# Kernel optimization log

Hardware: AMD Instinct MI355X
Metric: run time of the kernel (lower is better)

## Reference

```python
import jax, jax.numpy as jnp
import numpy as np


def setup_inputs() -> dict:
    key = jax.random.key(0)
    k1, k2 = jax.random.split(key, 2)
    N, HrWr, HW = 16, 4096, 1024
    num_levels, max_k = 3, 5
    return {
        "R_combined": jax.random.normal(k1, (N, HrWr, HW), dtype=jnp.float32),
        "k_logits": jax.random.normal(k2, (num_levels, max_k), dtype=jnp.float32),
        "temperature": jnp.array(1.0, dtype=jnp.float32),
        "max_k": 5,
        "num_levels": 3,
    }


def reference(R_combined, k_logits, temperature, max_k, num_levels):
    # --- gumbel-softmax over k choices (soft samples, as in F.gumbel_softmax) ---
    gkey = jax.random.key(42)
    u = jax.random.uniform(gkey, k_logits.shape, k_logits.dtype,
                           minval=1e-6, maxval=1.0 - 1e-6)
    gumbels = -jnp.log(-jnp.log(u))
    k_probs = jax.nn.softmax((k_logits + gumbels) / temperature, axis=-1)  # [L, max_k]
    k_hard = jnp.argmax(k_probs, axis=-1) + 1                              # [L] ints in [1, max_k]
    k_soft = jnp.sum(k_probs * jnp.arange(1, max_k + 1, dtype=k_probs.dtype), axis=-1)
    # straight-through estimator
    k_selected = (jax.lax.stop_gradient(k_hard.astype(k_soft.dtype))
                  + k_soft - jax.lax.stop_gradient(k_soft))

    # --- top-k over HrWr axis (dim=1); take max_k once, then per-level mask.
    # topk(k) + pad to max_k with (-inf, 0)  ==  topk(max_k) masked at rank >= k,
    # since top_k returns sorted-descending values (matches torch.topk sorted=True).
    x = jnp.swapaxes(R_combined, 1, 2)           # [N, HW, HrWr]
    vals, idx = jax.lax.top_k(x, max_k)          # [N, HW, max_k]
    vals = jnp.swapaxes(vals, 1, 2)              # [N, max_k, HW]
    idx = jnp.swapaxes(idx, 1, 2)                # [N, max_k, HW]

    rank = jnp.arange(max_k)                     # [max_k]
    mask = (rank[None, :] < k_hard[:, None])[:, None, :, None]  # [L, 1, max_k, 1]
    R_star_levels = jnp.where(mask, vals[None], -jnp.inf)       # [L, N, max_k, HW]
    R_idx_levels = jnp.where(mask, idx[None], 0)                # [L, N, max_k, HW]

    return (k_selected, R_star_levels, R_idx_levels)
```

## Files before the change

### kernel.cpp

```cpp
#include <hip/hip_runtime.h>
#include <math.h>
#include <float.h>
#include <stdint.h>

#define N_N   16
#define HRWR  4096
#define HW_   1024
#define LVLS  3
#define MAXK  5

#define SLICES   16
#define RSPLIT   8
#define K1_SEGS  4
#define K1_SEGLEN 128

#define NEG_SENTINEL (-1.0e30f)

__device__ __forceinline__ unsigned rotl32(unsigned x, unsigned r) {
  return (x << r) | (x >> (32u - r));
}

__device__ __forceinline__ bool beats(float v, int i, float V, int I) {
  return (v > V) || (v == V && i < I);
}

__global__ __launch_bounds__(256, 6)
void dynk_partial(const float* __restrict__ R, float2* __restrict__ ws)
{
  __shared__ float s_vals[K1_SEGS][64][MAXK];
  __shared__ int   s_idx [K1_SEGS][64][MAXK];

  const int tid   = threadIdx.x;
  const int c     = tid & 63;
  const int s     = tid >> 6;
  const int b     = blockIdx.x;
  const int rs    = b & (RSPLIT - 1);
  const int slice = (b >> 3) & (SLICES - 1);
  const int n     = b >> 7;

  const int r0 = rs * 512 + s * K1_SEGLEN;
  const float* __restrict__ base =
      R + ((size_t)n * HRWR + r0) * HW_ + slice * 64 + c;

  float tv[MAXK]; int ti[MAXK];
#pragma unroll
  for (int k = 0; k < MAXK; ++k) { tv[k] = -INFINITY; ti[k] = 0x7fffffff; }

  for (int r = 0; r < K1_SEGLEN; r += 8) {
    float v[8];
#pragma unroll
    for (int j = 0; j < 8; ++j) v[j] = base[(size_t)(r + j) * HW_];
#pragma unroll
    for (int j = 0; j < 8; ++j) {
      const float val = v[j];
      if (val > tv[MAXK - 1]) {
        tv[MAXK - 1] = val;
        ti[MAXK - 1] = r0 + r + j;
#pragma unroll
        for (int k = MAXK - 1; k > 0; --k) {
          if (tv[k] > tv[k - 1]) {
            float tf = tv[k]; tv[k] = tv[k - 1]; tv[k - 1] = tf;
            int   tt = ti[k]; ti[k] = ti[k - 1]; ti[k - 1] = tt;
          }
        }
      }
    }
  }

#pragma unroll
  for (int k = 0; k < MAXK; ++k) { s_vals[s][c][k] = tv[k]; s_idx[s][c][k] = ti[k]; }
  __syncthreads();

  if (tid < 64) {
    const int cc = tid;
    float fv[MAXK]; int fi[MAXK];
#pragma unroll
    for (int k = 0; k < MAXK; ++k) { fv[k] = s_vals[0][cc][k]; fi[k] = s_idx[0][cc][k]; }
    for (int ss = 1; ss < K1_SEGS; ++ss) {
#pragma unroll
      for (int k = 0; k < MAXK; ++k) {
        const float v = s_vals[ss][cc][k];
        const int   i = s_idx [ss][cc][k];
        if (beats(v, i, fv[MAXK - 1], fi[MAXK - 1])) {
          fv[MAXK - 1] = v; fi[MAXK - 1] = i;
#pragma unroll
          for (int k2 = MAXK - 1; k2 > 0; --k2) {
            if (beats(fv[k2], fi[k2], fv[k2 - 1], fi[k2 - 1])) {
              float tf = fv[k2]; fv[k2] = fv[k2 - 1]; fv[k2 - 1] = tf;
              int   tt = fi[k2]; fi[k2] = fi[k2 - 1]; fi[k2 - 1] = tt;
            }
          }
        }
      }
    }
    float2* __restrict__ dst = ws + ((size_t)b * 64 + cc) * MAXK;
#pragma unroll
    for (int k = 0; k < MAXK; ++k)
      dst[k] = make_float2(fv[k], __int_as_float(fi[k]));
  }
}

__global__ __launch_bounds__(256)
void dynk_final(const float2* __restrict__ ws,
                const float* __restrict__ k_logits,
                const float* __restrict__ temperature,
                float* __restrict__ out)
{
  __shared__ unsigned s_bits[LVLS * MAXK];
  __shared__ int      s_khard[LVLS];

  const int tid = threadIdx.x;

  if (tid < LVLS * MAXK) {
    unsigned x0 = 0u, x1 = (unsigned)tid;
    const unsigned k0 = 0u, k1 = 42u;
    const unsigned k2 = k0 ^ k1 ^ 0x1BD11BDAu;
    x0 += k0; x1 += k1;
#define TF_RND(rot) { x0 += x1; x1 = rotl32(x1, rot); x1 ^= x0; }
    TF_RND(13) TF_RND(15) TF_RND(26) TF_RND(6)  x0 += k1; x1 += k2 + 1u;
    TF_RND(17) TF_RND(29) TF_RND(16) TF_RND(24) x0 += k2; x1 += k0 + 2u;
    TF_RND(13) TF_RND(15) TF_RND(26) TF_RND(6)  x0 += k0; x1 += k1 + 3u;
    TF_RND(17) TF_RND(29) TF_RND(16) TF_RND(24) x0 += k1; x1 += k2 + 4u;
    TF_RND(13) TF_RND(15) TF_RND(26) TF_RND(6)  x0 += k2; x1 += k0 + 5u;
#undef TF_RND
    s_bits[tid] = x0 ^ x1;
  }
  __syncthreads();

  if (tid == 0) {
    const float T = temperature[0];
    for (int l = 0; l < LVLS; ++l) {
      float z[MAXK], p[MAXK];
      float zmax = -INFINITY;
      for (int k = 0; k < MAXK; ++k) {
        unsigned bits = s_bits[l * MAXK + k];
        float f = __uint_as_float((bits >> 9) | 0x3f800000u) - 1.0f;
        const float mn = 1e-6f;
        const float mx = 1.0f - 1e-6f;
        float u = fmaxf(mn, f * (mx - mn) + mn);
        float g = -logf(-logf(u));
        z[k] = (k_logits[l * MAXK + k] + g) / T;
        zmax = fmaxf(zmax, z[k]);
      }
      float sum = 0.0f;
      for (int k = 0; k < MAXK; ++k) { p[k] = expf(z[k] - zmax); sum += p[k]; }
      float pmax = -INFINITY; int arg = 0; float ksoft = 0.0f;
      for (int k = 0; k < MAXK; ++k) {
        p[k] = p[k] / sum;
        if (p[k] > pmax) { pmax = p[k]; arg = k; }
        ksoft += p[k] * (float)(k + 1);
      }
      const int khard = arg + 1;
      s_khard[l] = khard;
      if (blockIdx.x == 0) out[l] = ((float)khard + ksoft) - ksoft;
    }
  }
  __syncthreads();

  const int g  = blockIdx.x * 256 + tid;
  const int n  = g >> 10;
  const int hw = g & (HW_ - 1);
  const int slice = hw >> 6;
  const int cc    = hw & 63;

  const size_t lbase = (((size_t)n * SLICES + slice) * RSPLIT);

  float fv[MAXK]; int fi[MAXK];
  {
    const float2* __restrict__ src = ws + (lbase * 64 + cc) * MAXK;
#pragma unroll
    for (int k = 0; k < MAXK; ++k) {
      float2 e = src[k]; fv[k] = e.x; fi[k] = __float_as_int(e.y);
    }
  }
  for (int rs = 1; rs < RSPLIT; ++rs) {
    const float2* __restrict__ src = ws + (((lbase + rs) * 64) + cc) * MAXK;
#pragma unroll
    for (int k = 0; k < MAXK; ++k) {
      float2 e = src[k];
      const float v = e.x; const int i = __float_as_int(e.y);
      if (beats(v, i, fv[MAXK - 1], fi[MAXK - 1])) {
        fv[MAXK - 1] = v; fi[MAXK - 1] = i;
#pragma unroll
        for (int k2 = MAXK - 1; k2 > 0; --k2) {
          if (beats(fv[k2], fi[k2], fv[k2 - 1], fi[k2 - 1])) {
            float tf = fv[k2]; fv[k2] = fv[k2 - 1]; fv[k2 - 1] = tf;
            int   tt = fi[k2]; fi[k2] = fi[k2 - 1]; fi[k2 - 1] = tt;
          }
        }
      }
    }
  }

  float* __restrict__ star = out + LVLS;
  float* __restrict__ idxo = out + LVLS + (size_t)LVLS * N_N * MAXK * HW_;
#pragma unroll
  for (int l = 0; l < LVLS; ++l) {
    const int kh = s_khard[l];
#pragma unroll
    for (int k = 0; k < MAXK; ++k) {
      const bool on = (k < kh);
      const size_t off = (((size_t)l * N_N + n) * MAXK + k) * HW_ + hw;
      star[off] = on ? fv[k] : NEG_SENTINEL;
      idxo[off] = on ? (float)fi[k] : 0.0f;
    }
  }
}

extern "C" void kernel_launch(void* const* d_in, const int* in_sizes, int n_in,
                              void* d_out, int out_size, void* d_ws, size_t ws_size,
                              hipStream_t stream) {
  const float* R    = (const float*)d_in[0];
  const float* kl   = (const float*)d_in[1];
  const float* temp = (const float*)d_in[2];
  float* out  = (float*)d_out;
  float2* ws  = (float2*)d_ws;

  dynk_partial<<<dim3(N_N * SLICES * RSPLIT), dim3(256), 0, stream>>>(R, ws);
  dynk_final  <<<dim3((N_N * HW_) / 256), dim3(256), 0, stream>>>(ws, kl, temp, out);
}
```

Baseline: 410.6 us.

## Vectorize partial top-k with float4 columns and split final merge across four threads

The partial kernel now has each thread load float4 and keep four independent top-5 lists. Each block covers a full 1024-column row band of 64 rows, which drops the in-block shared-memory merge and the tail where only 64 threads were active. The final kernel merges 64 partial lists per column, split over 4 threads and combined in shared memory. The trade-offs are higher register pressure, more workspace traffic (64 splits instead of 8), and a scattered stride-5 float2 access pattern in the final kernel.

```diff
diff --git a/kernel.cpp b/kernel.cpp
--- a/kernel.cpp
+++ b/kernel.cpp
@@ -9,10 +9,12 @@
 #define LVLS  3
 #define MAXK  5
 
-#define SLICES   16
-#define RSPLIT   8
-#define K1_SEGS  4
-#define K1_SEGLEN 128
+#define SPLITS 64
+#define ROWS   (HRWR / SPLITS)
+#define CPT    4
+
+#define SUBS   4
+#define LPS    (SPLITS / SUBS)
 
 #define NEG_SENTINEL (-1.0e30f)
 
@@ -24,80 +26,57 @@
   return (v > V) || (v == V && i < I);
 }
 
-__global__ __launch_bounds__(256, 6)
-void dynk_partial(const float* __restrict__ R, float2* __restrict__ ws)
+__global__ __launch_bounds__(256, 4)
+void dynk_partial(const float4* __restrict__ R4, float2* __restrict__ ws)
 {
-  __shared__ float s_vals[K1_SEGS][64][MAXK];
-  __shared__ int   s_idx [K1_SEGS][64][MAXK];
-
-  const int tid   = threadIdx.x;
-  const int c     = tid & 63;
-  const int s     = tid >> 6;
-  const int b     = blockIdx.x;
-  const int rs    = b & (RSPLIT - 1);
-  const int slice = (b >> 3) & (SLICES - 1);
-  const int n     = b >> 7;
-
-  const int r0 = rs * 512 + s * K1_SEGLEN;
-  const float* __restrict__ base =
-      R + ((size_t)n * HRWR + r0) * HW_ + slice * 64 + c;
-
-  float tv[MAXK]; int ti[MAXK];
-#pragma unroll
-  for (int k = 0; k < MAXK; ++k) { tv[k] = -INFINITY; ti[k] = 0x7fffffff; }
-
-  for (int r = 0; r < K1_SEGLEN; r += 8) {
-    float v[8];
-#pragma unroll
-    for (int j = 0; j < 8; ++j) v[j] = base[(size_t)(r + j) * HW_];
-#pragma unroll
-    for (int j = 0; j < 8; ++j) {
-      const float val = v[j];
-      if (val > tv[MAXK - 1]) {
-        tv[MAXK - 1] = val;
-        ti[MAXK - 1] = r0 + r + j;
-#pragma unroll
-        for (int k = MAXK - 1; k > 0; --k) {
-          if (tv[k] > tv[k - 1]) {
-            float tf = tv[k]; tv[k] = tv[k - 1]; tv[k - 1] = tf;
-            int   tt = ti[k]; ti[k] = ti[k - 1]; ti[k - 1] = tt;
-          }
-        }
-      }
-    }
-  }
-
-#pragma unroll
-  for (int k = 0; k < MAXK; ++k) { s_vals[s][c][k] = tv[k]; s_idx[s][c][k] = ti[k]; }
-  __syncthreads();
-
-  if (tid < 64) {
-    const int cc = tid;
-    float fv[MAXK]; int fi[MAXK];
-#pragma unroll
-    for (int k = 0; k < MAXK; ++k) { fv[k] = s_vals[0][cc][k]; fi[k] = s_idx[0][cc][k]; }
-    for (int ss = 1; ss < K1_SEGS; ++ss) {
-#pragma unroll
-      for (int k = 0; k < MAXK; ++k) {
-        const float v = s_vals[ss][cc][k];
-        const int   i = s_idx [ss][cc][k];
-        if (beats(v, i, fv[MAXK - 1], fi[MAXK - 1])) {
-          fv[MAXK - 1] = v; fi[MAXK - 1] = i;
-#pragma unroll
-          for (int k2 = MAXK - 1; k2 > 0; --k2) {
-            if (beats(fv[k2], fi[k2], fv[k2 - 1], fi[k2 - 1])) {
-              float tf = fv[k2]; fv[k2] = fv[k2 - 1]; fv[k2 - 1] = tf;
-              int   tt = fi[k2]; fi[k2] = fi[k2 - 1]; fi[k2 - 1] = tt;
+  const int tid = threadIdx.x;
+  const int b   = blockIdx.x;
+  const int sp  = b & (SPLITS - 1);
+  const int n   = b >> 6;
+  const int r0  = sp * ROWS;
+
+  const float4* __restrict__ base =
+      R4 + ((size_t)n * HRWR + r0) * (HW_ / 4) + tid;
+
+  float tv[CPT][MAXK];
+  int   ti[CPT][MAXK];
+#pragma unroll
+  for (int cc = 0; cc < CPT; ++cc)
+#pragma unroll
+    for (int k = 0; k < MAXK; ++k) { tv[cc][k] = -INFINITY; ti[cc][k] = 0x7fffffff; }
+
+  for (int r = 0; r < ROWS; r += 4) {
+    float4 v[4];
+#pragma unroll
+    for (int j = 0; j < 4; ++j) v[j] = base[(size_t)(r + j) * (HW_ / 4)];
+#pragma unroll
+    for (int j = 0; j < 4; ++j) {
+      const float vals[CPT] = {v[j].x, v[j].y, v[j].z, v[j].w};
+      const int row = r0 + r + j;
+#pragma unroll
+      for (int cc = 0; cc < CPT; ++cc) {
+        const float val = vals[cc];
+        if (val > tv[cc][MAXK - 1]) {
+          tv[cc][MAXK - 1] = val;
+          ti[cc][MAXK - 1] = row;
+#pragma unroll
+          for (int k = MAXK - 1; k > 0; --k) {
+            if (tv[cc][k] > tv[cc][k - 1]) {
+              float tf = tv[cc][k]; tv[cc][k] = tv[cc][k - 1]; tv[cc][k - 1] = tf;
+              int   tt = ti[cc][k]; ti[cc][k] = ti[cc][k - 1]; ti[cc][k - 1] = tt;
             }
           }
         }
       }
     }
-    float2* __restrict__ dst = ws + ((size_t)b * 64 + cc) * MAXK;
+  }
+
+  float2* __restrict__ dst = ws + ((size_t)b * HW_ + (size_t)tid * CPT) * MAXK;
+#pragma unroll
+  for (int cc = 0; cc < CPT; ++cc)
 #pragma unroll
     for (int k = 0; k < MAXK; ++k)
-      dst[k] = make_float2(fv[k], __int_as_float(fi[k]));
-  }
+      dst[cc * MAXK + k] = make_float2(tv[cc][k], __int_as_float(ti[cc][k]));
 }
 
 __global__ __launch_bounds__(256)
@@ -108,6 +87,8 @@
 {
   __shared__ unsigned s_bits[LVLS * MAXK];
   __shared__ int      s_khard[LVLS];
+  __shared__ float    s_v[256][MAXK];
+  __shared__ int      s_i[256][MAXK];
 
   const int tid = threadIdx.x;
 
@@ -155,26 +136,21 @@
       if (blockIdx.x == 0) out[l] = ((float)khard + ksoft) - ksoft;
     }
   }
-  __syncthreads();
-
-  const int g  = blockIdx.x * 256 + tid;
-  const int n  = g >> 10;
-  const int hw = g & (HW_ - 1);
-  const int slice = hw >> 6;
-  const int cc    = hw & 63;
-
-  const size_t lbase = (((size_t)n * SLICES + slice) * RSPLIT);
+
+  const int g   = blockIdx.x * 256 + tid;
+  const int col = g >> 2;
+  const int sub = g & (SUBS - 1);
+  const int n   = col >> 10;
+  const int hw  = col & (HW_ - 1);
 
   float fv[MAXK]; int fi[MAXK];
-  {
-    const float2* __restrict__ src = ws + (lbase * 64 + cc) * MAXK;
-#pragma unroll
-    for (int k = 0; k < MAXK; ++k) {
-      float2 e = src[k]; fv[k] = e.x; fi[k] = __float_as_int(e.y);
-    }
-  }
-  for (int rs = 1; rs < RSPLIT; ++rs) {
-    const float2* __restrict__ src = ws + (((lbase + rs) * 64) + cc) * MAXK;
+#pragma unroll
+  for (int k = 0; k < MAXK; ++k) { fv[k] = -INFINITY; fi[k] = 0x7fffffff; }
+
+  for (int j = 0; j < LPS; ++j) {
+    const int sp = sub * LPS + j;
+    const float2* __restrict__ src =
+        ws + (((size_t)n * SPLITS + sp) * HW_ + hw) * MAXK;
 #pragma unroll
     for (int k = 0; k < MAXK; ++k) {
       float2 e = src[k];
@@ -192,17 +168,41 @@
     }
   }
 
-  float* __restrict__ star = out + LVLS;
-  float* __restrict__ idxo = out + LVLS + (size_t)LVLS * N_N * MAXK * HW_;
-#pragma unroll
-  for (int l = 0; l < LVLS; ++l) {
-    const int kh = s_khard[l];
-#pragma unroll
-    for (int k = 0; k < MAXK; ++k) {
-      const bool on = (k < kh);
-      const size_t off = (((size_t)l * N_N + n) * MAXK + k) * HW_ + hw;
-      star[off] = on ? fv[k] : NEG_SENTINEL;
-      idxo[off] = on ? (float)fi[k] : 0.0f;
+#pragma unroll
+  for (int k = 0; k < MAXK; ++k) { s_v[tid][k] = fv[k]; s_i[tid][k] = fi[k]; }
+  __syncthreads();
+
+  if (sub == 0) {
+    for (int s2 = 1; s2 < SUBS; ++s2) {
+#pragma unroll
+      for (int k = 0; k < MAXK; ++k) {
+        const float v = s_v[tid + s2][k];
+        const int   i = s_i[tid + s2][k];
+        if (beats(v, i, fv[MAXK - 1], fi[MAXK - 1])) {
+          fv[MAXK - 1] = v; fi[MAXK - 1] = i;
+#pragma unroll
+          for (int k2 = MAXK - 1; k2 > 0; --k2) {
+            if (beats(fv[k2], fi[k2], fv[k2 - 1], fi[k2 - 1])) {
+              float tf = fv[k2]; fv[k2] = fv[k2 - 1]; fv[k2 - 1] = tf;
+              int   tt = fi[k2]; fi[k2] = fi[k2 - 1]; fi[k2 - 1] = tt;
+            }
+          }
+        }
+      }
+    }
+
+    float* __restrict__ star = out + LVLS;
+    float* __restrict__ idxo = out + LVLS + (size_t)LVLS * N_N * MAXK * HW_;
+#pragma unroll
+    for (int l = 0; l < LVLS; ++l) {
+      const int kh = s_khard[l];
+#pragma unroll
+      for (int k = 0; k < MAXK; ++k) {
+        const bool on = (k < kh);
+        const size_t off = (((size_t)l * N_N + n) * MAXK + k) * HW_ + hw;
+        star[off] = on ? fv[k] : NEG_SENTINEL;
+        idxo[off] = on ? (float)fi[k] : 0.0f;
+      }
     }
   }
 }
@@ -210,12 +210,12 @@
 extern "C" void kernel_launch(void* const* d_in, const int* in_sizes, int n_in,
                               void* d_out, int out_size, void* d_ws, size_t ws_size,
                               hipStream_t stream) {
-  const float* R    = (const float*)d_in[0];
-  const float* kl   = (const float*)d_in[1];
+  const float4* R4  = (const float4*)d_in[0];
+  const float*  kl  = (const float*)d_in[1];
   const float* temp = (const float*)d_in[2];
-  float* out  = (float*)d_out;
+  float*  out = (float*)d_out;
   float2* ws  = (float2*)d_ws;
 
-  dynk_partial<<<dim3(N_N * SLICES * RSPLIT), dim3(256), 0, stream>>>(R, ws);
-  dynk_final  <<<dim3((N_N * HW_) / 256), dim3(256), 0, stream>>>(ws, kl, temp, out);
-}
+  dynk_partial<<<dim3(N_N * SPLITS), dim3(256), 0, stream>>>(R4, ws);
+  dynk_final  <<<dim3((N_N * HW_ * SUBS) / 256), dim3(256), 0, stream>>>(ws, kl, temp, out);
+}
```

After: 415.4 us. About the same (+1.2%).
